# Performance work log

Measured on AMD Instinct MI355X. Metric: run time of the kernel, lower is better.

## Reference

```python
import jax, jax.numpy as jnp
import numpy as np

N = 200000   # nodes
E = 6400000  # edges
F = 128      # input node features
H = 6        # hiddenSize (module constant)
C = 10       # num_classes
G = 64       # graphs in batch


def setup_inputs() -> dict:
    key = jax.random.key(0)
    ks = jax.random.split(key, 7)
    x = jax.random.normal(ks[0], (N, F), dtype=jnp.float32)
    edge_index = jax.random.randint(ks[1], (2, E), 0, N, dtype=jnp.int32)
    batch = jnp.sort(jax.random.randint(ks[2], (N,), 0, G, dtype=jnp.int32))
    W1 = jax.random.normal(ks[3], (F, H), dtype=jnp.float32) * (1.0 / np.sqrt(F))
    b1 = jnp.zeros((H,), dtype=jnp.float32)
    W2 = jax.random.normal(ks[4], (H, C), dtype=jnp.float32) * (1.0 / np.sqrt(H))
    b2 = jnp.zeros((C,), dtype=jnp.float32)
    return {"x": x, "edge_index": edge_index, "batch": batch,
            "W1": W1, "b1": b1, "W2": W2, "b2": b2}


def _gcn_conv(x, W, b, row, col, dis):
    # PyG GCNConv: h = x W; out = D^{-1/2}(A+I)D^{-1/2} h + b
    h = x @ W                                      # [N, out]
    norm = dis[row] * dis[col]                     # [E] edge normalization
    msg = norm[:, None] * h[row]                   # gather from source nodes
    agg = jax.ops.segment_sum(msg, col, num_segments=N)  # scatter-add to targets
    # self-loop term: norm = dis[i]*dis[i]
    return agg + (dis * dis)[:, None] * h + b


def reference(x, edge_index, batch, W1, b1, W2, b2):
    row, col = edge_index[0], edge_index[1]
    # degree after adding self-loops (edge_weight = 1)
    deg = jax.ops.segment_sum(jnp.ones((E,), dtype=x.dtype), col, num_segments=N) + 1.0
    dis = jax.lax.rsqrt(deg)                       # deg^{-1/2}

    h = _gcn_conv(x, W1, b1, row, col, dis)
    h = jax.nn.relu(h)
    # dropout is identity in inference mode
    h = _gcn_conv(h, W2, b2, row, col, dis)        # [N, C]

    # global mean pool over each graph
    sums = jax.ops.segment_sum(h, batch, num_segments=G)                  # [G, C]
    cnts = jax.ops.segment_sum(jnp.ones((N,), dtype=h.dtype), batch, num_segments=G)
    pooled = sums / jnp.maximum(cnts, 1.0)[:, None]
    return jax.nn.log_softmax(pooled, axis=1)      # [G, C]
```

## Files before the change

kernel.cpp:

```cpp
#include <hip/hip_runtime.h>
#include <math.h>

#define N_NODES 200000
#define N_EDGES 6400000
#define F_IN    128
#define H_HID   6
#define C_OUT   10
#define G_BATCH 64

#define TILE_E  8192
#define NT      ((N_EDGES + TILE_E - 1) / TILE_E)
#define EPT     16
#define BSH     9
#define BNODES  512
#define NBUCK   ((N_NODES + BNODES - 1) / BNODES)
#define BCAP    17408
#define XBLK    512
#define NXB     ((N_NODES + XBLK - 1) / XBLK)

__device__ __forceinline__ unsigned short f2bf(float f) {
    unsigned u = __float_as_uint(f);
    u += 0x7fff + ((u >> 16) & 1);
    return (unsigned short)(u >> 16);
}
__device__ __forceinline__ unsigned pack2(float a, float b) {
    return (unsigned)f2bf(a) | ((unsigned)f2bf(b) << 16);
}
__device__ __forceinline__ float bf_lo(unsigned u) { return __uint_as_float(u << 16); }
__device__ __forceinline__ float bf_hi(unsigned u) { return __uint_as_float(u & 0xffff0000u); }

__global__ __launch_bounds__(512, 8) void megaA_kernel(const int* __restrict__ row,
                                                       const int* __restrict__ col,
                                                       const float* __restrict__ x,
                                                       const float* __restrict__ W1,
                                                       int* __restrict__ gcur,
                                                       int* __restrict__ binned,
                                                       float* __restrict__ xacc, int E) {
    __shared__ int sortbuf[TILE_E];
    __shared__ int cnt[512];
    __shared__ int pos[513];
    __shared__ int lbase[512];
    __shared__ int wtot[8];
    int tid = threadIdx.x;

    if (blockIdx.x >= NT) {
        float* w = (float*)sortbuf;
        for (int i = tid; i < F_IN * H_HID; i += 512) w[i] = W1[i];
        __syncthreads();
        int n = (blockIdx.x - NT) * XBLK + tid;
        if (n >= N_NODES) return;
        float acc[H_HID] = {0.f, 0.f, 0.f, 0.f, 0.f, 0.f};
        const float4* xr = (const float4*)(x + (size_t)n * F_IN);
#pragma unroll 4
        for (int f4 = 0; f4 < F_IN / 4; ++f4) {
            float4 v = xr[f4];
            int f = f4 * 4;
#pragma unroll
            for (int j = 0; j < H_HID; ++j) {
                acc[j] += v.x * w[(f + 0) * H_HID + j] + v.y * w[(f + 1) * H_HID + j]
                        + v.z * w[(f + 2) * H_HID + j] + v.w * w[(f + 3) * H_HID + j];
            }
        }
#pragma unroll
        for (int j = 0; j < H_HID; ++j) xacc[j * N_NODES + n] = acc[j];
        return;
    }

    int t = blockIdx.x;
    int base = t * TILE_E;
    int tile_n = min(TILE_E, E - base);

    cnt[tid] = 0;
    __syncthreads();

    int myval[EPT];
    int myb[EPT];
    int ebase = base + tid * EPT;
    if (ebase + EPT <= E) {
        const int4* c4 = (const int4*)(col + ebase);
        const int4* r4 = (const int4*)(row + ebase);
#pragma unroll
        for (int q = 0; q < EPT / 4; ++q) {
            int4 c = c4[q];
            int4 r = r4[q];
            int k = q * 4;
            myval[k + 0] = ((c.x & (BNODES - 1)) << 18) | r.x;  myb[k + 0] = c.x >> BSH;
            myval[k + 1] = ((c.y & (BNODES - 1)) << 18) | r.y;  myb[k + 1] = c.y >> BSH;
            myval[k + 2] = ((c.z & (BNODES - 1)) << 18) | r.z;  myb[k + 2] = c.z >> BSH;
            myval[k + 3] = ((c.w & (BNODES - 1)) << 18) | r.w;  myb[k + 3] = c.w >> BSH;
        }
#pragma unroll
        for (int k = 0; k < EPT; ++k) atomicAdd(&cnt[myb[k]], 1);
    } else {
#pragma unroll
        for (int k = 0; k < EPT; ++k) {
            int e = ebase + k;
            if (e < E) {
                int c = col[e];
                myval[k] = ((c & (BNODES - 1)) << 18) | row[e];
                myb[k] = c >> BSH;
                atomicAdd(&cnt[myb[k]], 1);
            } else {
                myb[k] = -1;
            }
        }
    }
    __syncthreads();

    int c = cnt[tid];
    int v = c;
    int lane = tid & 63, wid = tid >> 6;
#pragma unroll
    for (int off = 1; off < 64; off <<= 1) {
        int u = __shfl_up(v, off);
        if (lane >= off) v += u;
    }
    if (lane == 63) wtot[wid] = v;
    __syncthreads();
    if (tid == 0) {
        int running = 0;
#pragma unroll
        for (int i = 0; i < 8; ++i) { int w2 = wtot[i]; wtot[i] = running; running += w2; }
    }
    __syncthreads();
    int incl = v + wtot[wid];
    int excl = incl - c;
    pos[tid] = excl;
    cnt[tid] = excl;
    if (tid == 511) pos[512] = incl;
    if (tid < NBUCK) {
        lbase[tid] = tid * BCAP + (c ? atomicAdd(&gcur[tid], c) : 0);
    }
    __syncthreads();

#pragma unroll
    for (int k = 0; k < EPT; ++k) {
        if (myb[k] >= 0) {
            int p = atomicAdd(&cnt[myb[k]], 1);
            sortbuf[p] = myval[k];
        }
    }
    __syncthreads();

    for (int i = tid; i < tile_n; i += 512) {
        int lo = 0, hi = NBUCK - 1;
        while (lo < hi) {
            int mid = (lo + hi + 1) >> 1;
            if (pos[mid] <= i) lo = mid; else hi = mid - 1;
        }
        binned[lbase[lo] + (i - pos[lo])] = sortbuf[i];
    }
}

__global__ __launch_bounds__(1024) void passB2_kernel(const int* __restrict__ gcur,
                                                      const int* __restrict__ binned,
                                                      const float* __restrict__ xacc,
                                                      uint4* __restrict__ h1b) {
    __shared__ int cnt[512];
    int b = blockIdx.x, tid = threadIdx.x;
    int bb = b * BCAP, be = bb + gcur[b];
    if (tid < 512) cnt[tid] = 0;
    __syncthreads();
    int e = bb + tid;
    for (; e + 3072 < be; e += 4096) {
        int p0 = binned[e], p1 = binned[e + 1024], p2 = binned[e + 2048], p3 = binned[e + 3072];
        atomicAdd(&cnt[p0 >> 18], 1); atomicAdd(&cnt[p1 >> 18], 1);
        atomicAdd(&cnt[p2 >> 18], 1); atomicAdd(&cnt[p3 >> 18], 1);
    }
    for (; e < be; e += 1024) atomicAdd(&cnt[binned[e] >> 18], 1);
    __syncthreads();
    if (tid < 512) {
        int n = (b << BSH) + tid;
        if (n < N_NODES) {
            float d = rsqrtf((float)cnt[tid] + 1.0f);
            float a0 = xacc[0 * N_NODES + n], a1 = xacc[1 * N_NODES + n];
            float a2 = xacc[2 * N_NODES + n], a3 = xacc[3 * N_NODES + n];
            float a4 = xacc[4 * N_NODES + n], a5 = xacc[5 * N_NODES + n];
            uint4 o;
            o.x = pack2(d * a0, d * a1);
            o.y = pack2(d * a2, d * a3);
            o.z = pack2(d * a4, d * a5);
            o.w = __float_as_uint(d);
            h1b[n] = o;
        }
    }
}

#define BG_SORT()                                                               \
    int bb = b * BCAP, be = bb + gcur[b];                                       \
    if (tid < 512) cnt[tid] = 0;                                                \
    __syncthreads();                                                            \
    {                                                                           \
        int e = bb + tid;                                                       \
        for (; e + 3072 < be; e += 4096) {                                      \
            int p0 = binned[e], p1 = binned[e + 1024];                          \
            int p2 = binned[e + 2048], p3 = binned[e + 3072];                   \
            atomicAdd(&cnt[p0 >> 18], 1); atomicAdd(&cnt[p1 >> 18], 1);         \
            atomicAdd(&cnt[p2 >> 18], 1); atomicAdd(&cnt[p3 >> 18], 1);         \
        }                                                                       \
        for (; e < be; e += 1024) atomicAdd(&cnt[binned[e] >> 18], 1);          \
    }                                                                           \
    __syncthreads();                                                            \
    {                                                                           \
        int v0 = (tid < 512) ? cnt[tid] : 0;                                    \
        int v = v0;                                                             \
        int lane = tid & 63, wid = tid >> 6;                                    \
        _Pragma("unroll")                                                       \
        for (int off = 1; off < 64; off <<= 1) {                                \
            int u = __shfl_up(v, off);                                          \
            if (lane >= off) v += u;                                            \
        }                                                                       \
        if (wid < 8 && lane == 63) wtot[wid] = v;                               \
        __syncthreads();                                                        \
        if (tid == 0) {                                                         \
            int running = 0;                                                    \
            _Pragma("unroll")                                                   \
            for (int i = 0; i < 8; ++i) { int w2 = wtot[i]; wtot[i] = running; running += w2; } \
        }                                                                       \
        __syncthreads();                                                        \
        if (tid < 512) cnt[tid] = v + wtot[wid] - v0;                           \
    }                                                                           \
    __syncthreads();                                                            \
    {                                                                           \
        int e = bb + tid;                                                       \
        for (; e + 3072 < be; e += 4096) {                                      \
            int p0 = binned[e], p1 = binned[e + 1024];                          \
            int p2 = binned[e + 2048], p3 = binned[e + 3072];                   \
            int s0 = atomicAdd(&cnt[p0 >> 18], 1); stage[s0] = p0 & 0x3FFFF;    \
            int s1 = atomicAdd(&cnt[p1 >> 18], 1); stage[s1] = p1 & 0x3FFFF;    \
            int s2 = atomicAdd(&cnt[p2 >> 18], 1); stage[s2] = p2 & 0x3FFFF;    \
            int s3 = atomicAdd(&cnt[p3 >> 18], 1); stage[s3] = p3 & 0x3FFFF;    \
        }                                                                       \
        for (; e < be; e += 1024) {                                             \
            int p = binned[e];                                                  \
            int s = atomicAdd(&cnt[p >> 18], 1); stage[s] = p & 0x3FFFF;        \
        }                                                                       \
    }                                                                           \
    __syncthreads();

#define GATHER_BODY(TBL)                                                        \
    float a[H_HID] = {0.f, 0.f, 0.f, 0.f, 0.f, 0.f};                            \
    {                                                                           \
        int ee = s + sub;                                                       \
        for (; ee + 24 < e_end; ee += 32) {                                     \
            int i0 = stage[ee], i1 = stage[ee + 8];                             \
            int i2 = stage[ee + 16], i3 = stage[ee + 24];                       \
            uint4 v0 = TBL[i0], v1 = TBL[i1], v2 = TBL[i2], v3 = TBL[i3];       \
            a[0] += (bf_lo(v0.x) + bf_lo(v1.x)) + (bf_lo(v2.x) + bf_lo(v3.x));  \
            a[1] += (bf_hi(v0.x) + bf_hi(v1.x)) + (bf_hi(v2.x) + bf_hi(v3.x));  \
            a[2] += (bf_lo(v0.y) + bf_lo(v1.y)) + (bf_lo(v2.y) + bf_lo(v3.y));  \
            a[3] += (bf_hi(v0.y) + bf_hi(v1.y)) + (bf_hi(v2.y) + bf_hi(v3.y));  \
            a[4] += (bf_lo(v0.z) + bf_lo(v1.z)) + (bf_lo(v2.z) + bf_lo(v3.z));  \
            a[5] += (bf_hi(v0.z) + bf_hi(v1.z)) + (bf_hi(v2.z) + bf_hi(v3.z));  \
        }                                                                       \
        for (; ee < e_end; ee += 8) {                                           \
            uint4 vv = TBL[stage[ee]];                                          \
            a[0] += bf_lo(vv.x); a[1] += bf_hi(vv.x);                           \
            a[2] += bf_lo(vv.y); a[3] += bf_hi(vv.y);                           \
            a[4] += bf_lo(vv.z); a[5] += bf_hi(vv.z);                           \
        }                                                                       \
    }                                                                           \
    _Pragma("unroll")                                                           \
    for (int j = 0; j < H_HID; ++j) {                                           \
        _Pragma("unroll")                                                       \
        for (int off = 4; off > 0; off >>= 1) a[j] += __shfl_xor(a[j], off);    \
    }

__global__ __launch_bounds__(1024) void bg1_kernel(const int* __restrict__ gcur,
                                                   const int* __restrict__ binned,
                                                   const uint4* __restrict__ h1b,
                                                   const float* __restrict__ b1,
                                                   uint4* __restrict__ rs) {
    __shared__ int stage[BCAP];
    __shared__ int cnt[512];
    __shared__ int wtot[8];
    int b = blockIdx.x, tid = threadIdx.x;
    BG_SORT()

    int sub = tid & 7, grp = tid >> 3;
    for (int ch = 0; ch < 4; ++ch) {
        int ln = ch * 128 + grp;
        int n = (b << BSH) + ln;
        int s = ln ? cnt[ln - 1] : 0;
        int e_end = cnt[ln];
        GATHER_BODY(h1b)
        if (sub == 0 && n < N_NODES) {
            uint4 self = h1b[n];
            float d = __uint_as_float(self.w);
            float sf[H_HID] = {bf_lo(self.x), bf_hi(self.x), bf_lo(self.y),
                               bf_hi(self.y), bf_lo(self.z), bf_hi(self.z)};
            float r[H_HID];
#pragma unroll
            for (int j = 0; j < H_HID; ++j) {
                float vv = d * (a[j] + sf[j]) + b1[j];
                r[j] = d * (vv > 0.f ? vv : 0.f);
            }
            uint4 o;
            o.x = pack2(r[0], r[1]);
            o.y = pack2(r[2], r[3]);
            o.z = pack2(r[4], r[5]);
            o.w = self.w;
            rs[n] = o;
        }
    }
}

__global__ __launch_bounds__(1024) void bg2_kernel(const int* __restrict__ gcur,
                                                   const int* __restrict__ binned,
                                                   const uint4* __restrict__ rs,
                                                   const float* __restrict__ W2,
                                                   const int* __restrict__ batch,
                                                   float* __restrict__ sums) {
    __shared__ int stage[BCAP];
    __shared__ int cnt[512];
    __shared__ int wtot[8];
    __shared__ float w2s[H_HID * C_OUT];
    __shared__ float nv[128][C_OUT + 1];
    __shared__ int lg[128];
    __shared__ float gacc[2][C_OUT];
    __shared__ int sg0;
    int b = blockIdx.x, tid = threadIdx.x;
    if (tid < H_HID * C_OUT) w2s[tid] = W2[tid];
    if (tid < 2 * C_OUT) ((float*)gacc)[tid] = 0.f;
    if (tid == 0) sg0 = batch[b << BSH];
    BG_SORT()

    int sub = tid & 7, grp = tid >> 3;
    for (int ch = 0; ch < 4; ++ch) {
        int ln = ch * 128 + grp;
        int n = (b << BSH) + ln;
        int s = ln ? cnt[ln - 1] : 0;
        int e_end = cnt[ln];
        GATHER_BODY(rs)
        uint4 self = {0u, 0u, 0u, 0u};
        if (n < N_NODES) self = rs[n];
        float d = (n < N_NODES) ? __uint_as_float(self.w) : 0.f;
        float t[H_HID] = {a[0] + bf_lo(self.x), a[1] + bf_hi(self.x),
                          a[2] + bf_lo(self.y), a[3] + bf_hi(self.y),
                          a[4] + bf_lo(self.z), a[5] + bf_hi(self.z)};
        {
            float accv = 0.f;
#pragma unroll
            for (int j = 0; j < H_HID; ++j) accv += t[j] * w2s[j * C_OUT + sub];
            nv[grp][sub] = d * accv;
            if (sub < 2) {
                float accv2 = 0.f;
#pragma unroll
                for (int j = 0; j < H_HID; ++j) accv2 += t[j] * w2s[j * C_OUT + sub + 8];
                nv[grp][sub + 8] = d * accv2;
            }
        }
        if (sub == 0) lg[grp] = (n < N_NODES) ? batch[n] : sg0;
        __syncthreads();
        if (tid < 80) {
            int seg = tid / C_OUT, cc = tid - seg * C_OUT;
            int g = -1; float av = 0.f;
            for (int i = 0; i < 16; ++i) {
                int wdx = seg * 16 + i;
                int gw = lg[wdx];
                if (gw != g) {
                    if (g >= 0) {
                        int r2 = g - sg0;
                        if (r2 < 2) atomicAdd(&gacc[r2][cc], av);
                        else atomicAdd(&sums[g * C_OUT + cc], av);
                    }
                    g = gw; av = 0.f;
                }
                av += nv[wdx][cc];
            }
            int r2 = g - sg0;
            if (r2 < 2) atomicAdd(&gacc[r2][cc], av);
            else atomicAdd(&sums[g * C_OUT + cc], av);
        }
        __syncthreads();
    }
    if (tid < 2 * C_OUT) {
        int r2 = tid / C_OUT, cc = tid - r2 * C_OUT;
        int g = sg0 + r2;
        if (g < G_BATCH) atomicAdd(&sums[g * C_OUT + cc], gacc[r2][cc]);
    }
}

__global__ void pool_finish_kernel(const float* __restrict__ sums, const int* __restrict__ batch,
                                   const float* __restrict__ b2, float* __restrict__ out) {
    int g = threadIdx.x;
    if (g >= G_BATCH) return;
    int lo = 0, hi = N_NODES;
    while (lo < hi) { int mid = (lo + hi) >> 1; if (batch[mid] < g) lo = mid + 1; else hi = mid; }
    int c0 = lo;
    hi = N_NODES;
    while (lo < hi) { int mid = (lo + hi) >> 1; if (batch[mid] < g + 1) lo = mid + 1; else hi = mid; }
    float inv = 1.0f / fmaxf((float)(lo - c0), 1.0f);
    float v[C_OUT], m = -INFINITY;
#pragma unroll
    for (int c = 0; c < C_OUT; ++c) {
        v[c] = sums[g * C_OUT + c] * inv + b2[c];
        m = fmaxf(m, v[c]);
    }
    float s = 0.f;
#pragma unroll
    for (int c = 0; c < C_OUT; ++c) s += expf(v[c] - m);
    float lse = m + logf(s);
#pragma unroll
    for (int c = 0; c < C_OUT; ++c) out[g * C_OUT + c] = v[c] - lse;
}

extern "C" void kernel_launch(void* const* d_in, const int* in_sizes, int n_in,
                              void* d_out, int out_size, void* d_ws, size_t ws_size,
                              hipStream_t stream) {
    const float* x   = (const float*)d_in[0];
    const int* ei    = (const int*)d_in[1];
    const int* row   = ei;
    const int* col   = ei + N_EDGES;
    const int* batch = (const int*)d_in[2];
    const float* W1  = (const float*)d_in[3];
    const float* b1  = (const float*)d_in[4];
    const float* W2  = (const float*)d_in[5];
    const float* b2  = (const float*)d_in[6];
    float* out = (float*)d_out;

    char* p = (char*)d_ws;
    float* sums   = (float*)p;  p += (size_t)G_BATCH * C_OUT * 4;
    int*   gcur   = (int*)p;    p += (size_t)400 * 4;
    int*   binned = (int*)p;    p += (size_t)NBUCK * BCAP * 4;
    float* xacc   = (float*)p;  p += (size_t)H_HID * N_NODES * 4;
    uint4* h1b    = (uint4*)p;  p += (size_t)N_NODES * 16;
    uint4* rs     = (uint4*)p;

    hipMemsetAsync(sums, 0, (size_t)G_BATCH * C_OUT * 4 + 400 * 4, stream);

    megaA_kernel  <<<NT + NXB, 512, 0, stream>>>(row, col, x, W1, gcur, binned, xacc, N_EDGES);
    passB2_kernel <<<NBUCK, 1024, 0, stream>>>(gcur, binned, xacc, h1b);
    bg1_kernel    <<<NBUCK, 1024, 0, stream>>>(gcur, binned, h1b, b1, rs);
    bg2_kernel    <<<NBUCK, 1024, 0, stream>>>(gcur, binned, rs, W2, batch, sums);
    pool_finish_kernel<<<1, 64, 0, stream>>>(sums, batch, b2, out);
}
```

Baseline: 319.6 us.

## Cache per-node degrees and bucket-sorted CSR to skip repeated in-block sorting

passB2 now writes the per-node in-degree counts to global memory, so bg1 and bg2 no longer recount the bucket's edges with shared-memory atomics. bg1 performs the counting sort once, using the stored degrees for the prefix scan, and writes the sorted source indices out as a CSR array. bg2 then loads that CSR slice with vectorized copies instead of sorting again. The cost is an extra global write and read of the sorted edge array plus a degree array, in exchange for removing two histogram passes and one scatter-sort pass.

Result: no change. 318.0 us (median of 2 runs) (-0.5%).

```diff
diff --git a/kernel.cpp b/kernel.cpp
--- a/kernel.cpp
+++ b/kernel.cpp
@@ -155,6 +155,7 @@
 __global__ __launch_bounds__(1024) void passB2_kernel(const int* __restrict__ gcur,
                                                       const int* __restrict__ binned,
                                                       const float* __restrict__ xacc,
+                                                      int* __restrict__ deg,
                                                       uint4* __restrict__ h1b) {
     __shared__ int cnt[512];
     int b = blockIdx.x, tid = threadIdx.x;
@@ -172,7 +173,9 @@
     if (tid < 512) {
         int n = (b << BSH) + tid;
         if (n < N_NODES) {
-            float d = rsqrtf((float)cnt[tid] + 1.0f);
+            int dv = cnt[tid];
+            deg[n] = dv;
+            float d = rsqrtf((float)dv + 1.0f);
             float a0 = xacc[0 * N_NODES + n], a1 = xacc[1 * N_NODES + n];
             float a2 = xacc[2 * N_NODES + n], a3 = xacc[3 * N_NODES + n];
             float a4 = xacc[4 * N_NODES + n], a5 = xacc[5 * N_NODES + n];
@@ -186,23 +189,10 @@
     }
 }
 
-#define BG_SORT()                                                               \
-    int bb = b * BCAP, be = bb + gcur[b];                                       \
-    if (tid < 512) cnt[tid] = 0;                                                \
-    __syncthreads();                                                            \
+#define DEG_SCAN(INCL)                                                          \
     {                                                                           \
-        int e = bb + tid;                                                       \
-        for (; e + 3072 < be; e += 4096) {                                      \
-            int p0 = binned[e], p1 = binned[e + 1024];                          \
-            int p2 = binned[e + 2048], p3 = binned[e + 3072];                   \
-            atomicAdd(&cnt[p0 >> 18], 1); atomicAdd(&cnt[p1 >> 18], 1);         \
-            atomicAdd(&cnt[p2 >> 18], 1); atomicAdd(&cnt[p3 >> 18], 1);         \
-        }                                                                       \
-        for (; e < be; e += 1024) atomicAdd(&cnt[binned[e] >> 18], 1);          \
-    }                                                                           \
-    __syncthreads();                                                            \
-    {                                                                           \
-        int v0 = (tid < 512) ? cnt[tid] : 0;                                    \
+        int n0 = (b << BSH) + tid;                                              \
+        int v0 = (tid < 512 && n0 < N_NODES) ? deg[n0] : 0;                     \
         int v = v0;                                                             \
         int lane = tid & 63, wid = tid >> 6;                                    \
         _Pragma("unroll")                                                       \
@@ -218,23 +208,7 @@
             for (int i = 0; i < 8; ++i) { int w2 = wtot[i]; wtot[i] = running; running += w2; } \
         }                                                                       \
         __syncthreads();                                                        \
-        if (tid < 512) cnt[tid] = v + wtot[wid] - v0;                           \
-    }                                                                           \
-    __syncthreads();                                                            \
-    {                                                                           \
-        int e = bb + tid;                                                       \
-        for (; e + 3072 < be; e += 4096) {                                      \
-            int p0 = binned[e], p1 = binned[e + 1024];                          \
-            int p2 = binned[e + 2048], p3 = binned[e + 3072];                   \
-            int s0 = atomicAdd(&cnt[p0 >> 18], 1); stage[s0] = p0 & 0x3FFFF;    \
-            int s1 = atomicAdd(&cnt[p1 >> 18], 1); stage[s1] = p1 & 0x3FFFF;    \
-            int s2 = atomicAdd(&cnt[p2 >> 18], 1); stage[s2] = p2 & 0x3FFFF;    \
-            int s3 = atomicAdd(&cnt[p3 >> 18], 1); stage[s3] = p3 & 0x3FFFF;    \
-        }                                                                       \
-        for (; e < be; e += 1024) {                                             \
-            int p = binned[e];                                                  \
-            int s = atomicAdd(&cnt[p >> 18], 1); stage[s] = p & 0x3FFFF;        \
-        }                                                                       \
+        if (tid < 512) cnt[tid] = v + wtot[wid] - (INCL ? 0 : v0);              \
     }                                                                           \
     __syncthreads();
 
@@ -268,14 +242,43 @@
 
 __global__ __launch_bounds__(1024) void bg1_kernel(const int* __restrict__ gcur,
                                                    const int* __restrict__ binned,
+                                                   const int* __restrict__ deg,
                                                    const uint4* __restrict__ h1b,
                                                    const float* __restrict__ b1,
+                                                   int* __restrict__ csr,
                                                    uint4* __restrict__ rs) {
     __shared__ int stage[BCAP];
     __shared__ int cnt[512];
     __shared__ int wtot[8];
     int b = blockIdx.x, tid = threadIdx.x;
-    BG_SORT()
+    int bb = b * BCAP, be = bb + gcur[b];
+    int total = be - bb;
+
+    DEG_SCAN(0)
+
+    {
+        int e = bb + tid;
+        for (; e + 3072 < be; e += 4096) {
+            int p0 = binned[e], p1 = binned[e + 1024];
+            int p2 = binned[e + 2048], p3 = binned[e + 3072];
+            int s0 = atomicAdd(&cnt[p0 >> 18], 1); stage[s0] = p0 & 0x3FFFF;
+            int s1 = atomicAdd(&cnt[p1 >> 18], 1); stage[s1] = p1 & 0x3FFFF;
+            int s2 = atomicAdd(&cnt[p2 >> 18], 1); stage[s2] = p2 & 0x3FFFF;
+            int s3 = atomicAdd(&cnt[p3 >> 18], 1); stage[s3] = p3 & 0x3FFFF;
+        }
+        for (; e < be; e += 1024) {
+            int p = binned[e];
+            int s = atomicAdd(&cnt[p >> 18], 1); stage[s] = p & 0x3FFFF;
+        }
+    }
+    __syncthreads();
+
+    for (int i = tid * 4; i + 3 < total; i += 4096)
+        *(int4*)(csr + bb + i) = *(const int4*)(stage + i);
+    {
+        int b4 = total & ~3, r = total - b4;
+        if (tid < r) csr[bb + b4 + tid] = stage[b4 + tid];
+    }
 
     int sub = tid & 7, grp = tid >> 3;
     for (int ch = 0; ch < 4; ++ch) {
@@ -306,7 +309,8 @@
 }
 
 __global__ __launch_bounds__(1024) void bg2_kernel(const int* __restrict__ gcur,
-                                                   const int* __restrict__ binned,
+                                                   const int* __restrict__ deg,
+                                                   const int* __restrict__ csr,
                                                    const uint4* __restrict__ rs,
                                                    const float* __restrict__ W2,
                                                    const int* __restrict__ batch,
@@ -320,10 +324,20 @@
     __shared__ float gacc[2][C_OUT];
     __shared__ int sg0;
     int b = blockIdx.x, tid = threadIdx.x;
+    int bb = b * BCAP;
+    int total = gcur[b];
     if (tid < H_HID * C_OUT) w2s[tid] = W2[tid];
     if (tid < 2 * C_OUT) ((float*)gacc)[tid] = 0.f;
     if (tid == 0) sg0 = batch[b << BSH];
-    BG_SORT()
+
+    for (int i = tid * 4; i + 3 < total; i += 4096)
+        *(int4*)(stage + i) = *(const int4*)(csr + bb + i);
+    {
+        int b4 = total & ~3, r = total - b4;
+        if (tid < r) stage[b4 + tid] = csr[bb + b4 + tid];
+    }
+
+    DEG_SCAN(1)
 
     int sub = tid & 7, grp = tid >> 3;
     for (int ch = 0; ch < 4; ++ch) {
@@ -422,7 +436,9 @@
     char* p = (char*)d_ws;
     float* sums   = (float*)p;  p += (size_t)G_BATCH * C_OUT * 4;
     int*   gcur   = (int*)p;    p += (size_t)400 * 4;
+    int*   deg    = (int*)p;    p += (size_t)N_NODES * 4;
     int*   binned = (int*)p;    p += (size_t)NBUCK * BCAP * 4;
+    int*   csr    = (int*)p;    p += (size_t)NBUCK * BCAP * 4;
     float* xacc   = (float*)p;  p += (size_t)H_HID * N_NODES * 4;
     uint4* h1b    = (uint4*)p;  p += (size_t)N_NODES * 16;
     uint4* rs     = (uint4*)p;
@@ -430,8 +446,8 @@
     hipMemsetAsync(sums, 0, (size_t)G_BATCH * C_OUT * 4 + 400 * 4, stream);
 
     megaA_kernel  <<<NT + NXB, 512, 0, stream>>>(row, col, x, W1, gcur, binned, xacc, N_EDGES);
-    passB2_kernel <<<NBUCK, 1024, 0, stream>>>(gcur, binned, xacc, h1b);
-    bg1_kernel    <<<NBUCK, 1024, 0, stream>>>(gcur, binned, h1b, b1, rs);
-    bg2_kernel    <<<NBUCK, 1024, 0, stream>>>(gcur, binned, rs, W2, batch, sums);
+    passB2_kernel <<<NBUCK, 1024, 0, stream>>>(gcur, binned, xacc, deg, h1b);
+    bg1_kernel    <<<NBUCK, 1024, 0, stream>>>(gcur, binned, deg, h1b, b1, csr, rs);
+    bg2_kernel    <<<NBUCK, 1024, 0, stream>>>(gcur, deg, csr, rs, W2, batch, sums);
     pool_finish_kernel<<<1, 64, 0, stream>>>(sums, batch, b2, out);
 }
```
